# Kernel optimization log

Hardware: AMD Instinct MI355X
Metric: run time of the kernel (lower is better)

The kernel has to match this reference:

```python
import jax, jax.numpy as jnp
import numpy as np
import math

D_MODEL = 2048
NUM_HEADS = 16
HEAD_DIM = D_MODEL // NUM_HEADS  # 128
B, S = 2, 2048


def setup_inputs() -> dict:
    key = jax.random.key(0)
    ks = jax.random.split(key, 11)
    s_in = 1.0 / math.sqrt(D_MODEL)
    return {
        "query": jax.random.normal(ks[0], (B, S, D_MODEL), dtype=jnp.float32),
        "key": jax.random.normal(ks[1], (B, S, D_MODEL), dtype=jnp.float32),
        "value": jax.random.normal(ks[2], (B, S, D_MODEL), dtype=jnp.float32),
        "Wq": jax.random.normal(ks[3], (D_MODEL, D_MODEL), dtype=jnp.float32) * s_in,
        "bq": jnp.zeros((D_MODEL,), dtype=jnp.float32),
        "Wk": jax.random.normal(ks[4], (D_MODEL, HEAD_DIM), dtype=jnp.float32) * s_in,
        "bk": jnp.zeros((HEAD_DIM,), dtype=jnp.float32),
        "Wv": jax.random.normal(ks[5], (D_MODEL, HEAD_DIM), dtype=jnp.float32) * s_in,
        "bv": jnp.zeros((HEAD_DIM,), dtype=jnp.float32),
        "Wo": jax.random.normal(ks[6], (D_MODEL, D_MODEL), dtype=jnp.float32) * s_in,
        "bo": jnp.zeros((D_MODEL,), dtype=jnp.float32),
    }


def reference(query, key, value, Wq, bq, Wk, bk, Wv, bv, Wo, bo):
    b, s, d_model = query.shape
    h, d = NUM_HEADS, HEAD_DIM
    # Projections: Q has h heads, K/V have a single shared head (MQA)
    Q = (query @ Wq + bq).reshape(b, s, h, d).transpose(0, 2, 1, 3)  # [b,h,s,d]
    K = key @ Wk + bk      # [b,s,d]
    V = value @ Wv + bv    # [b,s,d]
    scale = 1.0 / math.sqrt(d)
    # broadcast single K head over all h query heads
    scores = jnp.einsum('bhqd,bkd->bhqk', Q, K) * scale  # [b,h,s,s]
    weights = jax.nn.softmax(scores, axis=-1)
    attn = jnp.einsum('bhqk,bkd->bhqd', weights, V)      # [b,h,s,d]
    attn = attn.transpose(0, 2, 1, 3).reshape(b, s, d_model)
    return attn @ Wo + bo
```

## Files before the change

kernel.cpp:

```cpp
#include <hip/hip_runtime.h>


typedef unsigned short u16;
typedef __attribute__((ext_vector_type(8))) short bf16x8;
typedef __attribute__((ext_vector_type(4))) short bf16x4;
typedef __attribute__((ext_vector_type(4))) float f32x4;

#define D_MODEL 2048
#define SEQ     2048
#define NH      16
#define HD      128
#define BK      32

__device__ __forceinline__ u16 f2bf(float f){
  union { float f; unsigned u; } v; v.f = f;
  unsigned r = (v.u + 0x7FFFu + ((v.u >> 16) & 1u)) >> 16;
  return (u16)r;
}

#if __has_builtin(__builtin_amdgcn_cvt_pk_bf16_f32)
__device__ __forceinline__ unsigned pack2bf(float a, float b){
  auto v = __builtin_amdgcn_cvt_pk_bf16_f32(a, b);
  unsigned u; __builtin_memcpy(&u, &v, 4); return u;
}
#else
__device__ __forceinline__ unsigned pack2bf(float a, float b){
  return (unsigned)f2bf(a) | ((unsigned)f2bf(b) << 16);
}
#endif

__device__ __forceinline__ void gll16(const void* g, void* l){
  __builtin_amdgcn_global_load_lds(
      (const __attribute__((address_space(1))) void*)g,
      (__attribute__((address_space(3))) void*)l, 16, 0, 0);
}

__global__ __launch_bounds__(256) void convert3_kernel(
    const float4* __restrict__ a, const float4* __restrict__ b, const float4* __restrict__ c,
    ushort4* __restrict__ oa, ushort4* __restrict__ ob, ushort4* __restrict__ oc){
  int i = blockIdx.x*256 + threadIdx.x;
  float4 va = a[i], vb = b[i], vc = c[i];
  ushort4 ra, rb, rc;
  ra.x=f2bf(va.x); ra.y=f2bf(va.y); ra.z=f2bf(va.z); ra.w=f2bf(va.w);
  rb.x=f2bf(vb.x); rb.y=f2bf(vb.y); rb.z=f2bf(vb.z); rb.w=f2bf(vb.w);
  rc.x=f2bf(vc.x); rc.y=f2bf(vc.y); rc.z=f2bf(vc.z); rc.w=f2bf(vc.w);
  oa[i]=ra; ob[i]=rb; oc[i]=rc;
}

__global__ __launch_bounds__(256) void transpose_all(
    const float* __restrict__ Wq, const float* __restrict__ Wo,
    const float* __restrict__ Wk, const float* __restrict__ Wv,
    u16* __restrict__ WqT, u16* __restrict__ WoT,
    u16* __restrict__ WkT, u16* __restrict__ WvT){
  __shared__ float tt[32][33];
  int id = blockIdx.x;
  const float* in; u16* outp; int C, bx, by;
  if (id < 4096)      { in=Wq; outp=WqT; C=2048; bx=id&63;        by=id>>6; }
  else if (id < 8192) { id-=4096; in=Wo; outp=WoT; C=2048; bx=id&63; by=id>>6; }
  else if (id < 8448) { id-=8192; in=Wk; outp=WkT; C=128;  bx=id&3;  by=id>>2; }
  else                { id-=8448; in=Wv; outp=WvT; C=128;  bx=id&3;  by=id>>2; }
  const int R = 2048;
  int c0 = bx*32, r0 = by*32;
  int tx = threadIdx.x & 31, ty = threadIdx.x >> 5;
  #pragma unroll
  for (int k=0;k<4;k++) tt[ty+k*8][tx] = in[(size_t)(r0+ty+k*8)*C + c0+tx];
  __syncthreads();
  #pragma unroll
  for (int k=0;k<4;k++) outp[(size_t)(c0+ty+k*8)*R + r0+tx] = f2bf(tt[tx][ty+k*8]);
}

__device__ __forceinline__ void gemm_core_db(
    const u16* __restrict__ A, const u16* __restrict__ BT,
    int lda, int ldb, int m0, int n0, int kbeg, int kend,
    u16* As, u16* Bs, f32x4 acc[4][4])
{
  const int t = threadIdx.x;
  const int w = t >> 6, l = t & 63;
  const int wr = w >> 1, wc = w & 1;
  const int c16 = l & 15, q = l >> 4;
  const int srow = l >> 2;
  const int sc   = ((l & 3) ^ ((l >> 3) & 3)) * 8;

  int aoff[4], boff[4];
  #pragma unroll
  for (int mt=0;mt<4;mt++){
    int row = wr*64 + mt*16 + c16;
    aoff[mt] = row*BK + ((q ^ ((row>>1)&3))*8);
  }
  #pragma unroll
  for (int nt=0;nt<4;nt++){
    int row = wc*64 + nt*16 + c16;
    boff[nt] = row*BK + ((q ^ ((row>>1)&3))*8);
  }

  auto issue = [&](int k0, int buf){
    u16* Ad = As + buf*4096;
    u16* Bd = Bs + buf*4096;
    #pragma unroll
    for (int half=0; half<2; half++){
      int r = half*64 + w*16 + srow;
      gll16(A  + (size_t)(m0+r)*lda + k0 + sc, Ad + (half*64 + w*16)*BK);
      gll16(BT + (size_t)(n0+r)*ldb + k0 + sc, Bd + (half*64 + w*16)*BK);
    }
  };

  const int n = (kend - kbeg) / BK;
  issue(kbeg, 0);
  for (int i = 0; i < n; i++){
    __syncthreads();
    if (i+1 < n) issue(kbeg + (i+1)*BK, (i+1)&1);
    const u16* Ab = As + (i&1)*4096;
    const u16* Bb = Bs + (i&1)*4096;
    bf16x8 af[4], bfr[4];
    #pragma unroll
    for (int mt=0;mt<4;mt++) af[mt]  = *(const bf16x8*)(Ab + aoff[mt]);
    #pragma unroll
    for (int nt=0;nt<4;nt++) bfr[nt] = *(const bf16x8*)(Bb + boff[nt]);
    #pragma unroll
    for (int mt=0;mt<4;mt++)
      #pragma unroll
      for (int nt=0;nt<4;nt++)
        acc[mt][nt] = __builtin_amdgcn_mfma_f32_16x16x32_bf16(af[mt], bfr[nt], acc[mt][nt], 0,0,0);
  }
}

__global__ __launch_bounds__(256) void proj_kernel(
    const u16* __restrict__ qb, const u16* __restrict__ kb, const u16* __restrict__ vb,
    const u16* __restrict__ WqT, const u16* __restrict__ WkT, const u16* __restrict__ WvT,
    const float* __restrict__ bq, u16* __restrict__ Qp, float* __restrict__ part)
{
  __shared__ u16 As[2*4096], Bs[2*4096];
  f32x4 acc[4][4];
  f32x4 z = {0.f,0.f,0.f,0.f};
  #pragma unroll
  for (int i=0;i<4;i++) for (int j=0;j<4;j++) acc[i][j] = z;
  const int t = threadIdx.x, w = t>>6, l = t&63, wr = w>>1, wc = w&1, c16 = l&15, q = l>>4;
  int id = blockIdx.x;
  if (id < 512){
    int m0 = (id & 31)*128, n0 = (id >> 5)*128;
    gemm_core_db(qb, WqT, 2048, 2048, m0, n0, 0, 2048, As, Bs, acc);
    #pragma unroll
    for (int mt=0;mt<4;mt++)
      #pragma unroll
      for (int nt=0;nt<4;nt++){
        int col = n0 + wc*64 + nt*16 + c16;
        float bv = bq[col];
        #pragma unroll
        for (int r=0;r<4;r++){
          int row = m0 + wr*64 + mt*16 + q*4 + r;
          Qp[(size_t)row*D_MODEL + col] = f2bf(acc[mt][nt][r] + bv);
        }
      }
  } else {
    int kvid = id - 512;
    int zi = kvid & 3, nb = (kvid >> 2) & 1, mi = kvid >> 3;
    const u16* Am = nb ? vb  : kb;
    const u16* Bm = nb ? WvT : WkT;
    gemm_core_db(Am, Bm, 2048, 2048, mi*128, 0, zi*512, zi*512+512, As, Bs, acc);
    float* dst = part + (size_t)(zi*2 + nb)*524288;
    #pragma unroll
    for (int mt=0;mt<4;mt++)
      #pragma unroll
      for (int nt=0;nt<4;nt++){
        int col = wc*64 + nt*16 + c16;
        #pragma unroll
        for (int r=0;r<4;r++){
          int row = mi*128 + wr*64 + mt*16 + q*4 + r;
          dst[(size_t)row*128 + col] = acc[mt][nt][r];
        }
      }
  }
}

__global__ __launch_bounds__(256) void oproj_kernel(
    const u16* __restrict__ A, const u16* __restrict__ BT, const float* __restrict__ bias,
    float* __restrict__ C)
{
  __shared__ u16 As[2*4096], Bs[2*4096];
  f32x4 acc[4][4];
  f32x4 z = {0.f,0.f,0.f,0.f};
  #pragma unroll
  for (int i=0;i<4;i++) for (int j=0;j<4;j++) acc[i][j] = z;
  int m0 = blockIdx.x*128, n0 = blockIdx.y*128;
  gemm_core_db(A, BT, 2048, 2048, m0, n0, 0, 2048, As, Bs, acc);
  const int t = threadIdx.x, w = t>>6, l = t&63, wr = w>>1, wc = w&1, c16 = l&15, q = l>>4;
  #pragma unroll
  for (int mt=0;mt<4;mt++)
    #pragma unroll
    for (int nt=0;nt<4;nt++){
      int col = n0 + wc*64 + nt*16 + c16;
      float bv = bias[col];
      #pragma unroll
      for (int r=0;r<4;r++){
        int row = m0 + wr*64 + mt*16 + q*4 + r;
        C[(size_t)row*D_MODEL + col] = acc[mt][nt][r] + bv;
      }
    }
}

__global__ __launch_bounds__(256) void kv_reduce_kernel(
    const float* __restrict__ part, const float* __restrict__ bk, const float* __restrict__ bv,
    u16* __restrict__ Kp, u16* __restrict__ VpT){
  int idx = blockIdx.x*256 + threadIdx.x;
  int d = idx & 127, sg = idx >> 7;
  float ka = 0.f, va = 0.f;
  #pragma unroll
  for (int zi=0; zi<4; zi++){
    ka += part[(size_t)(zi*2+0)*524288 + idx];
    va += part[(size_t)(zi*2+1)*524288 + idx];
  }
  Kp[idx] = f2bf(ka + bk[d]);
  int b = sg >> 11, sl = sg & 2047;
  VpT[(size_t)b*262144 + (size_t)d*2048 + sl] = f2bf(va + bv[d]);
}

__global__ __launch_bounds__(512, 2) void attn_kernel(
    const u16* __restrict__ Qp, const u16* __restrict__ Kp,
    const u16* __restrict__ VpT, u16* __restrict__ attnb){
  __shared__ u16 lds[65536];
  const int t = threadIdx.x;
  const int w = t >> 6, l = t & 63;
  const int c16 = l & 15, q = l >> 4;

  const int qt = blockIdx.x;
  const int bh = blockIdx.y;
  const int b = bh >> 4, h = bh & 15;

  const u16* Qbase = Qp  + ((size_t)(b*SEQ + qt*256 + w*32))*D_MODEL + h*HD;
  const u16* Kbase = Kp  + (size_t)(b*SEQ)*HD;
  const u16* Vbase = VpT + (size_t)b*HD*SEQ;

  const int sr = w*4 + (l >> 4);
  #pragma unroll
  for (int j=0;j<4;j++){
    int r = j*32 + sr;
    int g = (l & 15) ^ (r & 15);
    gll16(Kbase + (size_t)r*HD + g*8, lds + j*4096 + w*512);
  }
  #pragma unroll
  for (int j=0;j<4;j++){
    int d = j*32 + sr;
    int g = (l & 15) ^ (d & 15);
    gll16(Vbase + (size_t)d*SEQ + g*8, lds + 32768 + j*4096 + w*512);
  }
  bf16x8 qf[2][4];
  #pragma unroll
  for (int qs=0;qs<2;qs++)
    #pragma unroll
    for (int kk=0;kk<4;kk++)
      qf[qs][kk] = *(const bf16x8*)(Qbase + (size_t)(qs*16 + c16)*D_MODEL + (kk*4 + q)*8);
  __syncthreads();

  f32x4 o[2][8];
  f32x4 z4 = {0.f,0.f,0.f,0.f};
  #pragma unroll
  for (int qs=0;qs<2;qs++) for (int dt=0;dt<8;dt++) o[qs][dt] = z4;
  float mrow[2] = {-1e30f, -1e30f};
  float lrow[2] = {0.f, 0.f};
  const float cs = 0.08838834764831845f * 1.4426950408889634f;

  for (int kt = 0; kt < 16; kt++){
    const int p = kt & 1;
    if (kt < 15){
      u16* Kd = lds + (p^1)*16384;
      u16* Vd = lds + 32768 + (p^1)*16384;
      #pragma unroll
      for (int j=0;j<4;j++){
        int r = j*32 + sr;
        int g = (l & 15) ^ (r & 15);
        gll16(Kbase + (size_t)((kt+1)*128 + r)*HD + g*8, Kd + j*4096 + w*512);
      }
      #pragma unroll
      for (int j=0;j<4;j++){
        int d = j*32 + sr;
        int g = (l & 15) ^ (d & 15);
        gll16(Vbase + (size_t)d*SEQ + (kt+1)*128 + g*8, Vd + j*4096 + w*512);
      }
    }
    const u16* Ks = lds + p*16384;
    const u16* Vs = lds + 32768 + p*16384;

    f32x4 s[2][8];
    #pragma unroll
    for (int qs=0;qs<2;qs++) for (int kt8=0;kt8<8;kt8++) s[qs][kt8] = z4;
    __builtin_amdgcn_s_setprio(1);
    #pragma unroll
    for (int kt8=0; kt8<8; kt8++){
      #pragma unroll
      for (int kk=0;kk<4;kk++){
        int ch = kk*4 + q;
        bf16x8 kf = *(const bf16x8*)(Ks + (kt8*16 + c16)*128 + ((ch ^ c16) & 15)*8);
        s[0][kt8] = __builtin_amdgcn_mfma_f32_16x16x32_bf16(kf, qf[0][kk], s[0][kt8], 0,0,0);
        s[1][kt8] = __builtin_amdgcn_mfma_f32_16x16x32_bf16(kf, qf[1][kk], s[1][kt8], 0,0,0);
      }
    }
    __builtin_amdgcn_s_setprio(0);

    float alpha[2];
    #pragma unroll
    for (int qs=0; qs<2; qs++){
      float x[8];
      #pragma unroll
      for (int kt8=0;kt8<8;kt8++)
        x[kt8] = fmaxf(fmaxf(s[qs][kt8][0],s[qs][kt8][1]), fmaxf(s[qs][kt8][2],s[qs][kt8][3]));
      float vmax = fmaxf(fmaxf(fmaxf(x[0],x[1]),fmaxf(x[2],x[3])),
                         fmaxf(fmaxf(x[4],x[5]),fmaxf(x[6],x[7])));
      vmax = fmaxf(vmax, __shfl_xor(vmax, 16));
      vmax = fmaxf(vmax, __shfl_xor(vmax, 32));
      float mnew = fmaxf(mrow[qs], vmax);
      alpha[qs] = exp2f((mrow[qs] - mnew)*cs);
      float mc = mnew*cs;
      float rs[8];
      #pragma unroll
      for (int kt8=0;kt8<8;kt8++){
        float p0 = exp2f(__builtin_fmaf(s[qs][kt8][0], cs, -mc));
        float p1 = exp2f(__builtin_fmaf(s[qs][kt8][1], cs, -mc));
        float p2 = exp2f(__builtin_fmaf(s[qs][kt8][2], cs, -mc));
        float p3 = exp2f(__builtin_fmaf(s[qs][kt8][3], cs, -mc));
        s[qs][kt8][0]=p0; s[qs][kt8][1]=p1; s[qs][kt8][2]=p2; s[qs][kt8][3]=p3;
        rs[kt8] = (p0+p1)+(p2+p3);
      }
      float rsum = ((rs[0]+rs[1])+(rs[2]+rs[3])) + ((rs[4]+rs[5])+(rs[6]+rs[7]));
      rsum += __shfl_xor(rsum, 16);
      rsum += __shfl_xor(rsum, 32);
      lrow[qs] = lrow[qs]*alpha[qs] + rsum;
      mrow[qs] = mnew;
    }

    unsigned long long allone = __ballot(alpha[0] == 1.f && alpha[1] == 1.f);
    if (allone != ~0ull){
      #pragma unroll
      for (int qs=0;qs<2;qs++)
        #pragma unroll
        for (int dt=0;dt<8;dt++)
          #pragma unroll
          for (int r=0;r<4;r++) o[qs][dt][r] *= alpha[qs];
    }

    union PU { unsigned u[4]; bf16x8 v; } P32[2][4];
    #pragma unroll
    for (int qs=0;qs<2;qs++)
      #pragma unroll
      for (int kb=0;kb<4;kb++){
        P32[qs][kb].u[0] = pack2bf(s[qs][2*kb][0],   s[qs][2*kb][1]);
        P32[qs][kb].u[1] = pack2bf(s[qs][2*kb][2],   s[qs][2*kb][3]);
        P32[qs][kb].u[2] = pack2bf(s[qs][2*kb+1][0], s[qs][2*kb+1][1]);
        P32[qs][kb].u[3] = pack2bf(s[qs][2*kb+1][2], s[qs][2*kb+1][3]);
      }

    __builtin_amdgcn_s_setprio(1);
    #pragma unroll
    for (int kb=0; kb<4; kb++){
      int ca = 4*kb + (q>>1);
      int cb = ca + 2;
      #pragma unroll
      for (int dt=0; dt<8; dt++){
        int d = dt*16 + c16;
        union VU { bf16x4 h[2]; bf16x8 v; } vf;
        vf.h[0] = *(const bf16x4*)(Vs + d*128 + ((ca ^ c16) & 15)*8 + (q&1)*4);
        vf.h[1] = *(const bf16x4*)(Vs + d*128 + ((cb ^ c16) & 15)*8 + (q&1)*4);
        o[0][dt] = __builtin_amdgcn_mfma_f32_16x16x32_bf16(vf.v, P32[0][kb].v, o[0][dt], 0,0,0);
        o[1][dt] = __builtin_amdgcn_mfma_f32_16x16x32_bf16(vf.v, P32[1][kb].v, o[1][dt], 0,0,0);
      }
    }
    __builtin_amdgcn_s_setprio(0);
    __syncthreads();
  }

  #pragma unroll
  for (int qs=0;qs<2;qs++){
    float inv = 1.f / lrow[qs];
    int qrow = qt*256 + w*32 + qs*16 + c16;
    u16* dst = attnb + ((size_t)(b*SEQ) + qrow)*D_MODEL + h*HD + q*4;
    #pragma unroll
    for (int dt=0;dt<8;dt++){
      ushort4 pk;
      pk.x = f2bf(o[qs][dt][0]*inv);
      pk.y = f2bf(o[qs][dt][1]*inv);
      pk.z = f2bf(o[qs][dt][2]*inv);
      pk.w = f2bf(o[qs][dt][3]*inv);
      *(ushort4*)(dst + dt*16) = pk;
    }
  }
}

extern "C" void kernel_launch(void* const* d_in, const int* in_sizes, int n_in,
                              void* d_out, int out_size, void* d_ws, size_t ws_size,
                              hipStream_t stream) {
  (void)in_sizes; (void)n_in; (void)out_size; (void)ws_size;
  const float* query = (const float*)d_in[0];
  const float* key   = (const float*)d_in[1];
  const float* value = (const float*)d_in[2];
  const float* Wq    = (const float*)d_in[3];
  const float* bq    = (const float*)d_in[4];
  const float* Wk    = (const float*)d_in[5];
  const float* bk    = (const float*)d_in[6];
  const float* Wv    = (const float*)d_in[7];
  const float* bv    = (const float*)d_in[8];
  const float* Wo    = (const float*)d_in[9];
  const float* bo    = (const float*)d_in[10];
  float* out = (float*)d_out;

  char* W = (char*)d_ws;
  u16*  qb     = (u16*) (W + 0);
  u16*  kb     = (u16*) (W + 16777216);
  u16*  vb     = (u16*) (W + 33554432);
  u16*  WqT    = (u16*) (W + 50331648);
  u16*  WoT    = (u16*) (W + 58720256);
  u16*  WkT    = (u16*) (W + 67108864);
  u16*  WvT    = (u16*) (W + 67633152);
  u16*  Qp     = (u16*) (W + 68157440);
  u16*  Kp     = (u16*) (W + 84934656);
  u16*  VpT    = (u16*) (W + 85983232);
  u16*  attnb  = (u16*) (W + 87031808);
  float* kvpart= (float*)(W + 103809024);

  convert3_kernel<<<8192, 256, 0, stream>>>(
      (const float4*)query, (const float4*)key, (const float4*)value,
      (ushort4*)qb, (ushort4*)kb, (ushort4*)vb);
  transpose_all<<<8704, 256, 0, stream>>>(Wq, Wo, Wk, Wv, WqT, WoT, WkT, WvT);
  proj_kernel<<<768, 256, 0, stream>>>(qb, kb, vb, WqT, WkT, WvT, bq, Qp, kvpart);
  kv_reduce_kernel<<<2048, 256, 0, stream>>>(kvpart, bk, bv, Kp, VpT);
  attn_kernel<<<dim3(8,32), 512, 0, stream>>>(Qp, Kp, VpT, attnb);
  oproj_kernel<<<dim3(32,16), 256, 0, stream>>>(attnb, WoT, bo, out);
}
```

Before: 411.8 us.

## Fuse prep kernels, swizzle GEMM tile order, add lazy softmax rescale

Merges the input bf16 conversion and the weight transpose into a single prep launch, removing one kernel launch and its tail. Remaps the GEMM block indices in both the Q projection and the output projection so that blocks sharing weight columns run at the same time, which should improve L2 reuse. In attention, the first QK MFMA starts from zero instead of clearing the accumulators. The online-softmax rescale of the output now runs only when the row max grows by more than a threshold, with fewer shuffles and multiplies in exchange for exponentials that can reach up to 2^8 before normalisation. That exponent growth raises the risk of overflow and bf16 precision loss in P.

New measurement: 406.9 us. About the same (-1.2%).

```diff
diff --git a/kernel.cpp b/kernel.cpp
--- a/kernel.cpp
+++ b/kernel.cpp
@@ -35,25 +35,26 @@
       (__attribute__((address_space(3))) void*)l, 16, 0, 0);
 }
 
-__global__ __launch_bounds__(256) void convert3_kernel(
-    const float4* __restrict__ a, const float4* __restrict__ b, const float4* __restrict__ c,
-    ushort4* __restrict__ oa, ushort4* __restrict__ ob, ushort4* __restrict__ oc){
-  int i = blockIdx.x*256 + threadIdx.x;
-  float4 va = a[i], vb = b[i], vc = c[i];
-  ushort4 ra, rb, rc;
-  ra.x=f2bf(va.x); ra.y=f2bf(va.y); ra.z=f2bf(va.z); ra.w=f2bf(va.w);
-  rb.x=f2bf(vb.x); rb.y=f2bf(vb.y); rb.z=f2bf(vb.z); rb.w=f2bf(vb.w);
-  rc.x=f2bf(vc.x); rc.y=f2bf(vc.y); rc.z=f2bf(vc.z); rc.w=f2bf(vc.w);
-  oa[i]=ra; ob[i]=rb; oc[i]=rc;
-}
-
-__global__ __launch_bounds__(256) void transpose_all(
+__global__ __launch_bounds__(256) void prep_kernel(
+    const float4* __restrict__ qa, const float4* __restrict__ ka, const float4* __restrict__ va,
+    ushort4* __restrict__ oq, ushort4* __restrict__ ok, ushort4* __restrict__ ov,
     const float* __restrict__ Wq, const float* __restrict__ Wo,
     const float* __restrict__ Wk, const float* __restrict__ Wv,
     u16* __restrict__ WqT, u16* __restrict__ WoT,
     u16* __restrict__ WkT, u16* __restrict__ WvT){
   __shared__ float tt[32][33];
-  int id = blockIdx.x;
+  int bid = blockIdx.x;
+  if (bid < 8192){
+    int i = bid*256 + threadIdx.x;
+    float4 a = qa[i], b = ka[i], c = va[i];
+    ushort4 ra, rb, rc;
+    ra.x=f2bf(a.x); ra.y=f2bf(a.y); ra.z=f2bf(a.z); ra.w=f2bf(a.w);
+    rb.x=f2bf(b.x); rb.y=f2bf(b.y); rb.z=f2bf(b.z); rb.w=f2bf(b.w);
+    rc.x=f2bf(c.x); rc.y=f2bf(c.y); rc.z=f2bf(c.z); rc.w=f2bf(c.w);
+    oq[i]=ra; ok[i]=rb; ov[i]=rc;
+    return;
+  }
+  int id = bid - 8192;
   const float* in; u16* outp; int C, bx, by;
   if (id < 4096)      { in=Wq; outp=WqT; C=2048; bx=id&63;        by=id>>6; }
   else if (id < 8192) { id-=4096; in=Wo; outp=WoT; C=2048; bx=id&63; by=id>>6; }
@@ -137,7 +138,8 @@
   const int t = threadIdx.x, w = t>>6, l = t&63, wr = w>>1, wc = w&1, c16 = l&15, q = l>>4;
   int id = blockIdx.x;
   if (id < 512){
-    int m0 = (id & 31)*128, n0 = (id >> 5)*128;
+    int x = id & 7, j = id >> 3;
+    int m0 = (x*4 + (j & 3))*128, n0 = (j >> 2)*128;
     gemm_core_db(qb, WqT, 2048, 2048, m0, n0, 0, 2048, As, Bs, acc);
     #pragma unroll
     for (int mt=0;mt<4;mt++)
@@ -181,7 +183,9 @@
   f32x4 z = {0.f,0.f,0.f,0.f};
   #pragma unroll
   for (int i=0;i<4;i++) for (int j=0;j<4;j++) acc[i][j] = z;
-  int m0 = blockIdx.x*128, n0 = blockIdx.y*128;
+  int id = blockIdx.x;
+  int x = id & 7, j = id >> 3;
+  int m0 = (x*4 + (j & 3))*128, n0 = (j >> 2)*128;
   gemm_core_db(A, BT, 2048, 2048, m0, n0, 0, 2048, As, Bs, acc);
   const int t = threadIdx.x, w = t>>6, l = t&63, wr = w>>1, wc = w&1, c16 = l&15, q = l>>4;
   #pragma unroll
@@ -281,13 +285,16 @@
     const u16* Vs = lds + 32768 + p*16384;
 
     f32x4 s[2][8];
-    #pragma unroll
-    for (int qs=0;qs<2;qs++) for (int kt8=0;kt8<8;kt8++) s[qs][kt8] = z4;
     __builtin_amdgcn_s_setprio(1);
     #pragma unroll
     for (int kt8=0; kt8<8; kt8++){
-      #pragma unroll
-      for (int kk=0;kk<4;kk++){
+      {
+        bf16x8 kf = *(const bf16x8*)(Ks + (kt8*16 + c16)*128 + ((q ^ c16) & 15)*8);
+        s[0][kt8] = __builtin_amdgcn_mfma_f32_16x16x32_bf16(kf, qf[0][0], z4, 0,0,0);
+        s[1][kt8] = __builtin_amdgcn_mfma_f32_16x16x32_bf16(kf, qf[1][0], z4, 0,0,0);
+      }
+      #pragma unroll
+      for (int kk=1;kk<4;kk++){
         int ch = kk*4 + q;
         bf16x8 kf = *(const bf16x8*)(Ks + (kt8*16 + c16)*128 + ((ch ^ c16) & 15)*8);
         s[0][kt8] = __builtin_amdgcn_mfma_f32_16x16x32_bf16(kf, qf[0][kk], s[0][kt8], 0,0,0);
@@ -296,21 +303,37 @@
     }
     __builtin_amdgcn_s_setprio(0);
 
-    float alpha[2];
+    float vmax[2];
     #pragma unroll
     for (int qs=0; qs<2; qs++){
-      float x[8];
+      float xx[8];
       #pragma unroll
       for (int kt8=0;kt8<8;kt8++)
-        x[kt8] = fmaxf(fmaxf(s[qs][kt8][0],s[qs][kt8][1]), fmaxf(s[qs][kt8][2],s[qs][kt8][3]));
-      float vmax = fmaxf(fmaxf(fmaxf(x[0],x[1]),fmaxf(x[2],x[3])),
-                         fmaxf(fmaxf(x[4],x[5]),fmaxf(x[6],x[7])));
-      vmax = fmaxf(vmax, __shfl_xor(vmax, 16));
-      vmax = fmaxf(vmax, __shfl_xor(vmax, 32));
-      float mnew = fmaxf(mrow[qs], vmax);
-      alpha[qs] = exp2f((mrow[qs] - mnew)*cs);
-      float mc = mnew*cs;
-      float rs[8];
+        xx[kt8] = fmaxf(fmaxf(s[qs][kt8][0],s[qs][kt8][1]), fmaxf(s[qs][kt8][2],s[qs][kt8][3]));
+      float vm = fmaxf(fmaxf(fmaxf(xx[0],xx[1]),fmaxf(xx[2],xx[3])),
+                       fmaxf(fmaxf(xx[4],xx[5]),fmaxf(xx[6],xx[7])));
+      vm = fmaxf(vm, __shfl_xor(vm, 16));
+      vm = fmaxf(vm, __shfl_xor(vm, 32));
+      vmax[qs] = vm;
+    }
+    bool upd = ((vmax[0]-mrow[0])*cs > 8.f) || ((vmax[1]-mrow[1])*cs > 8.f);
+    if (__any(upd)){
+      #pragma unroll
+      for (int qs=0; qs<2; qs++){
+        float mnew = fmaxf(mrow[qs], vmax[qs]);
+        float a = exp2f((mrow[qs]-mnew)*cs);
+        mrow[qs] = mnew; lrow[qs] *= a;
+        #pragma unroll
+        for (int dt=0;dt<8;dt++)
+          #pragma unroll
+          for (int r=0;r<4;r++) o[qs][dt][r] *= a;
+      }
+    }
+    union PU { unsigned u[4]; bf16x8 v; } P32[2][4];
+    #pragma unroll
+    for (int qs=0; qs<2; qs++){
+      float mc = mrow[qs]*cs;
+      float rsum = 0.f;
       #pragma unroll
       for (int kt8=0;kt8<8;kt8++){
         float p0 = exp2f(__builtin_fmaf(s[qs][kt8][0], cs, -mc));
@@ -318,28 +341,11 @@
         float p2 = exp2f(__builtin_fmaf(s[qs][kt8][2], cs, -mc));
         float p3 = exp2f(__builtin_fmaf(s[qs][kt8][3], cs, -mc));
         s[qs][kt8][0]=p0; s[qs][kt8][1]=p1; s[qs][kt8][2]=p2; s[qs][kt8][3]=p3;
-        rs[kt8] = (p0+p1)+(p2+p3);
-      }
-      float rsum = ((rs[0]+rs[1])+(rs[2]+rs[3])) + ((rs[4]+rs[5])+(rs[6]+rs[7]));
+        rsum += (p0+p1)+(p2+p3);
+      }
       rsum += __shfl_xor(rsum, 16);
       rsum += __shfl_xor(rsum, 32);
-      lrow[qs] = lrow[qs]*alpha[qs] + rsum;
-      mrow[qs] = mnew;
-    }
-
-    unsigned long long allone = __ballot(alpha[0] == 1.f && alpha[1] == 1.f);
-    if (allone != ~0ull){
-      #pragma unroll
-      for (int qs=0;qs<2;qs++)
-        #pragma unroll
-        for (int dt=0;dt<8;dt++)
-          #pragma unroll
-          for (int r=0;r<4;r++) o[qs][dt][r] *= alpha[qs];
-    }
-
-    union PU { unsigned u[4]; bf16x8 v; } P32[2][4];
-    #pragma unroll
-    for (int qs=0;qs<2;qs++)
+      lrow[qs] += rsum;
       #pragma unroll
       for (int kb=0;kb<4;kb++){
         P32[qs][kb].u[0] = pack2bf(s[qs][2*kb][0],   s[qs][2*kb][1]);
@@ -347,6 +353,7 @@
         P32[qs][kb].u[2] = pack2bf(s[qs][2*kb+1][0], s[qs][2*kb+1][1]);
         P32[qs][kb].u[3] = pack2bf(s[qs][2*kb+1][2], s[qs][2*kb+1][3]);
       }
+    }
 
     __builtin_amdgcn_s_setprio(1);
     #pragma unroll
@@ -356,9 +363,9 @@
       #pragma unroll
       for (int dt=0; dt<8; dt++){
         int d = dt*16 + c16;
-        union VU { bf16x4 h[2]; bf16x8 v; } vf;
-        vf.h[0] = *(const bf16x4*)(Vs + d*128 + ((ca ^ c16) & 15)*8 + (q&1)*4);
-        vf.h[1] = *(const bf16x4*)(Vs + d*128 + ((cb ^ c16) & 15)*8 + (q&1)*4);
+        union VU { bf16x4 hh[2]; bf16x8 v; } vf;
+        vf.hh[0] = *(const bf16x4*)(Vs + d*128 + ((ca ^ c16) & 15)*8 + (q&1)*4);
+        vf.hh[1] = *(const bf16x4*)(Vs + d*128 + ((cb ^ c16) & 15)*8 + (q&1)*4);
         o[0][dt] = __builtin_amdgcn_mfma_f32_16x16x32_bf16(vf.v, P32[0][kb].v, o[0][dt], 0,0,0);
         o[1][dt] = __builtin_amdgcn_mfma_f32_16x16x32_bf16(vf.v, P32[1][kb].v, o[1][dt], 0,0,0);
       }
@@ -415,12 +422,12 @@
   u16*  attnb  = (u16*) (W + 87031808);
   float* kvpart= (float*)(W + 103809024);
 
-  convert3_kernel<<<8192, 256, 0, stream>>>(
+  prep_kernel<<<16896, 256, 0, stream>>>(
       (const float4*)query, (const float4*)key, (const float4*)value,
-      (ushort4*)qb, (ushort4*)kb, (ushort4*)vb);
-  transpose_all<<<8704, 256, 0, stream>>>(Wq, Wo, Wk, Wv, WqT, WoT, WkT, WvT);
+      (ushort4*)qb, (ushort4*)kb, (ushort4*)vb,
+      Wq, Wo, Wk, Wv, WqT, WoT, WkT, WvT);
   proj_kernel<<<768, 256, 0, stream>>>(qb, kb, vb, WqT, WkT, WvT, bq, Qp, kvpart);
   kv_reduce_kernel<<<2048, 256, 0, stream>>>(kvpart, bk, bv, Kp, VpT);
   attn_kernel<<<dim3(8,32), 512, 0, stream>>>(Qp, Kp, VpT, attnb);
-  oproj_kernel<<<dim3(32,16), 256, 0, stream>>>(attnb, WoT, bo, out);
-}
+  oproj_kernel<<<512, 256, 0, stream>>>(attnb, WoT, bo, out);
+}
```
